# Kernel tuning notes

Measured on AMD Instinct MI355X. Metric: run time of the kernel, lower is better.

## Reference

```python
import jax, jax.numpy as jnp
import numpy as np

N, E, DIN, D, H, L = 4096, 65536, 128, 256, 4, 3
DH = D // H


def _ln(x, g, b, eps=1e-5):
    m = jnp.mean(x, axis=-1, keepdims=True)
    v = jnp.mean((x - m) ** 2, axis=-1, keepdims=True)
    return (x - m) * jax.lax.rsqrt(v + eps) * g + b


def _gcn(x, w, b, row, col, n):
    # PyG GCNConv: add self-loops, symmetric normalization D^-1/2 A D^-1/2, aggregate at col (target)
    ar = jnp.arange(n, dtype=row.dtype)
    r = jnp.concatenate([row, ar])
    c = jnp.concatenate([col, ar])
    deg = jax.ops.segment_sum(jnp.ones(r.shape[0], x.dtype), c, num_segments=n)
    dinv = jnp.where(deg > 0, deg ** -0.5, 0.0)
    norm = dinv[r] * dinv[c]  # (E+N,)
    msg = x @ w.T  # (N, out)
    return jax.ops.segment_sum(norm[:, None] * msg[r], c, num_segments=n) + b


def setup_inputs() -> dict:
    key = jax.random.key(0)
    ks = jax.random.split(key, 12)
    rnd = lambda i, shape: jax.random.normal(ks[i], shape, jnp.float32) * 0.05
    return {
        "node_features": jax.random.normal(ks[0], (N, DIN), jnp.float32),
        "edge_index": jax.random.randint(ks[1], (2, E), 0, N, jnp.int32),
        "gcn1_w": rnd(2, (D, DIN)), "gcn1_b": jnp.zeros((D,), jnp.float32),
        "gcn2_w": rnd(3, (D, D)), "gcn2_b": jnp.zeros((D,), jnp.float32),
        "edge_w": rnd(4, (H, 3)), "edge_b": jnp.zeros((H,), jnp.float32),
        "proj_w": rnd(5, (D, DIN + D)), "proj_b": jnp.zeros((D,), jnp.float32),
        "wqkv": rnd(6, (L, 3 * D, D)), "bqkv": jnp.zeros((L, 3 * D), jnp.float32),
        "wo": rnd(7, (L, D, D)), "bo": jnp.zeros((L, D), jnp.float32),
        "ffn_w1": rnd(8, (L, 4 * D, D)), "ffn_b1": jnp.zeros((L, 4 * D), jnp.float32),
        "ffn_w2": rnd(9, (L, D, 4 * D)), "ffn_b2": jnp.zeros((L, D), jnp.float32),
        "ln1_g": jnp.ones((L, D), jnp.float32), "ln1_b": jnp.zeros((L, D), jnp.float32),
        "ln2_g": jnp.ones((L, D), jnp.float32), "ln2_b": jnp.zeros((L, D), jnp.float32),
        "out_w": rnd(10, (1, D)), "out_b": jnp.zeros((1,), jnp.float32),
    }


def reference(node_features, edge_index, gcn1_w, gcn1_b, gcn2_w, gcn2_b,
              edge_w, edge_b, proj_w, proj_b, wqkv, bqkv, wo, bo,
              ffn_w1, ffn_b1, ffn_w2, ffn_b2, ln1_g, ln1_b, ln2_g, ln2_b,
              out_w, out_b):
    n = node_features.shape[0]
    row, col = edge_index[0], edge_index[1]
    # two-layer GCN
    h = jax.nn.relu(_gcn(node_features, gcn1_w, gcn1_b, row, col, n))
    g = _gcn(h, gcn2_w, gcn2_b, row, col, n)
    x = jnp.concatenate([node_features, g], axis=-1) @ proj_w.T + proj_b  # (N, D)
    # edge-aware attention bias: per-edge linear+sigmoid scattered into dense (H, N, N)
    feat = jnp.stack([row.astype(x.dtype), col.astype(x.dtype),
                      jnp.ones(row.shape[0], x.dtype)], axis=-1)  # (E, 3)
    bpe = jax.nn.sigmoid(feat @ edge_w.T + edge_b)  # (E, H)
    bias = jnp.zeros((H, n, n), x.dtype).at[:, row, col].set(bpe.T)
    scale = 1.0 / np.sqrt(DH)
    for l in range(L):
        qkv = x @ wqkv[l].T + bqkv[l]
        q, k, v = jnp.split(qkv, 3, axis=-1)
        q = q.reshape(n, H, DH); k = k.reshape(n, H, DH); v = v.reshape(n, H, DH)
        s = jnp.einsum('nhd,mhd->hnm', q, k) * scale + bias
        a = jax.nn.softmax(s, axis=-1)
        o = jnp.einsum('hnm,mhd->nhd', a, v).reshape(n, D) @ wo[l].T + bo[l]
        x = _ln(x + o, ln1_g[l], ln1_b[l])
        f = jax.nn.relu(x @ ffn_w1[l].T + ffn_b1[l]) @ ffn_w2[l].T + ffn_b2[l]
        x = _ln(x + f, ln2_g[l], ln2_b[l])
    return jax.nn.sigmoid(x @ out_w.T + out_b)  # (N, 1) probs
```

## Files before the change

### kernel.cpp

```cpp
#include <hip/hip_runtime.h>
#include <math.h>

#define NN 4096
#define NE 65536
#define DIN 128
#define DM 256
#define NH 4
#define NL 3
#define NCH 4
#define TPC (NN / 64 / NCH)
#define NBKT 16384

typedef __attribute__((ext_vector_type(8))) short bf16x8;
typedef __attribute__((ext_vector_type(4))) float f32x4;

__device__ inline ushort f2b(float f) {
    union { float f; uint u; } v; v.f = f;
    uint r = v.u + 0x7fffu + ((v.u >> 16) & 1u);
    return (ushort)(r >> 16);
}

__device__ inline uint cvt_pk_bf16(float lo, float hi) {
    uint r;
    asm("v_cvt_pk_bf16_f32 %0, %1, %2" : "=v"(r) : "v"(lo), "v"(hi));
    return r;
}

__device__ inline void gl_lds16(const ushort* g, ushort* l) {
    __builtin_amdgcn_global_load_lds(
        (const __attribute__((address_space(1))) void*)g,
        (__attribute__((address_space(3))) void*)l, 16, 0, 0);
}


__global__ void k_edge1(const int* __restrict__ row, const int* __restrict__ col,
                        uint* __restrict__ bitmap, int* __restrict__ cnt_c,
                        int* __restrict__ bcnt, unsigned char* __restrict__ flag) {
    int e = blockIdx.x * 256 + threadIdx.x;
    if (e >= NE) return;
    int r = row[e], c = col[e];
    atomicAdd(&cnt_c[c], 1);
    uint idx = (uint)r * 4096u + (uint)c;
    uint m = 1u << (idx & 31);
    uint old = atomicOr(&bitmap[idx >> 5], m);
    int isnew = (old & m) ? 0 : 1;
    flag[e] = (unsigned char)isnew;
    if (isnew) atomicAdd(&bcnt[(r >> 4) * 64 + (c >> 6)], 1);
}

__global__ void k_edge2(const int* __restrict__ row, const int* __restrict__ col,
                        const unsigned char* __restrict__ flag,
                        const int* __restrict__ sc, int* __restrict__ fc, int* __restrict__ csc_row,
                        const int* __restrict__ bstart, int* __restrict__ bfill,
                        ushort* __restrict__ ents) {
    int e = blockIdx.x * 256 + threadIdx.x;
    if (e >= NE) return;
    int r = row[e], c = col[e];
    csc_row[sc[c] + atomicAdd(&fc[c], 1)] = r;
    if (flag[e]) {
        int key = (r >> 4) * 64 + (c >> 6);
        ents[bstart[key] + atomicAdd(&bfill[key], 1)] = (ushort)(((r & 15) << 6) | (c & 63));
    }
}

template <int N>
__global__ void k_scan(const int* __restrict__ cnt, int* __restrict__ start) {
    __shared__ int part[256];
    const int C = N / 256;
    int t = threadIdx.x;
    int s = 0;
    for (int i = 0; i < C; ++i) s += cnt[t * C + i];
    part[t] = s;
    __syncthreads();
    if (t == 0) {
        int acc = 0;
        for (int i = 0; i < 256; ++i) { int v = part[i]; part[i] = acc; acc += v; }
        start[N] = acc;
    }
    __syncthreads();
    int acc = part[t];
    for (int i = 0; i < C; ++i) { start[t * C + i] = acc; acc += cnt[t * C + i]; }
}

__global__ void k_dinv(const int* __restrict__ cnt_c, float* __restrict__ dinv) {
    int i = blockIdx.x * 256 + threadIdx.x;
    if (i < NN) dinv[i] = 1.0f / sqrtf((float)(cnt_c[i] + 1));
}

struct CvtP { const float* s[8]; ushort* d[8]; int n[8]; };
__global__ void k_cvt(CvtP p) {
    int y = blockIdx.y;
    int base = (blockIdx.x * 256 + threadIdx.x) * 4;
    if (base >= p.n[y]) return;
    float4 v = *(const float4*)(p.s[y] + base);
    float sc = 1.f;
    if (y == 1 && ((base >> 8) % 768) < 256) sc = 0.125f;
    ushort4 o;
    o.x = f2b(v.x * sc); o.y = f2b(v.y * sc); o.z = f2b(v.z * sc); o.w = f2b(v.w * sc);
    *(ushort4*)(p.d[y] + base) = o;
}

__global__ void k_scaleb(const float* __restrict__ b, float* __restrict__ o) {
    int i = blockIdx.x * 256 + threadIdx.x;
    if (i < NL * 768) o[i] = b[i] * (((i % 768) < 256) ? 0.125f : 1.f);
}

template <int FLAGS>
__global__ __launch_bounds__(256) void k_gemm_b(
    const ushort* __restrict__ A, int lda,
    const ushort* __restrict__ B, int ldb,
    float* __restrict__ Cf, ushort* __restrict__ Cb, int ldc,
    int K, const float* __restrict__ bias) {
    __shared__ ushort As[128 * 64];
    __shared__ ushort Bs[128 * 64];
    const int tid = threadIdx.x;
    const int w = tid >> 6, l = tid & 63;
    const int l15 = l & 15, l4 = l >> 4;
    const int row0 = blockIdx.y * 128, col0 = blockIdx.x * 128;
    const int wm = (w >> 1) * 64, wn = (w & 1) * 64;
    f32x4 acc[4][4];
#pragma unroll
    for (int i = 0; i < 4; ++i)
#pragma unroll
        for (int j = 0; j < 4; ++j) acc[i][j] = (f32x4){0.f, 0.f, 0.f, 0.f};
    for (int k0 = 0; k0 < K; k0 += 64) {
#pragma unroll
        for (int i = 0; i < 4; ++i) {
            int ci = tid + 256 * i;
            int r = ci >> 3, s = ci & 7;
            bf16x8 va = *(const bf16x8*)(A + (long)(row0 + r) * lda + k0 + s * 8);
            *(bf16x8*)&As[r * 64 + ((s ^ (r & 7)) * 8)] = va;
            bf16x8 vb = *(const bf16x8*)(B + (long)(col0 + r) * ldb + k0 + s * 8);
            *(bf16x8*)&Bs[r * 64 + ((s ^ (r & 7)) * 8)] = vb;
        }
        __syncthreads();
#pragma unroll
        for (int kk = 0; kk < 2; ++kk) {
            bf16x8 af[4], bfr[4];
#pragma unroll
            for (int i = 0; i < 4; ++i) {
                int ar = wm + i * 16 + l15;
                af[i] = *(const bf16x8*)&As[ar * 64 + (((kk * 4 + l4) ^ (ar & 7)) * 8)];
                int br = wn + i * 16 + l15;
                bfr[i] = *(const bf16x8*)&Bs[br * 64 + (((kk * 4 + l4) ^ (br & 7)) * 8)];
            }
#pragma unroll
            for (int i = 0; i < 4; ++i)
#pragma unroll
                for (int j = 0; j < 4; ++j)
                    acc[i][j] = __builtin_amdgcn_mfma_f32_16x16x32_bf16(af[i], bfr[j], acc[i][j], 0, 0, 0);
        }
        __syncthreads();
    }
#pragma unroll
    for (int i = 0; i < 4; ++i)
#pragma unroll
        for (int j = 0; j < 4; ++j) {
            int rb = row0 + wm + i * 16;
            int cb = col0 + wn + j * 16 + l15;
            float bv = bias ? bias[cb] : 0.f;
            if (FLAGS & 8) {
                ushort4 o4;
                o4.x = f2b(acc[i][j][0] + bv);
                o4.y = f2b(acc[i][j][1] + bv);
                o4.z = f2b(acc[i][j][2] + bv);
                o4.w = f2b(acc[i][j][3] + bv);
                *(ushort4*)(Cb + (long)cb * ldc + rb + l4 * 4) = o4;
            } else {
#pragma unroll
                for (int q = 0; q < 4; ++q) {
                    int r = rb + l4 * 4 + q;
                    float v = acc[i][j][q] + bv;
                    if (FLAGS & 4) v = fmaxf(v, 0.f);
                    if (FLAGS & 1) Cf[(long)r * ldc + cb] = v;
                    if (FLAGS & 2) Cb[(long)r * ldc + cb] = f2b(v);
                }
            }
        }
}

template <int ACT, int B16>
__global__ void k_gcn_agg(const float* __restrict__ msg, const int* __restrict__ sc,
                          const int* __restrict__ csc_row, const float* __restrict__ dinv,
                          const float* __restrict__ bias,
                          float* __restrict__ outf, ushort* __restrict__ outb) {
    int j = blockIdx.x;
    int d = threadIdx.x;
    float acc = 0.f;
    int a = sc[j], b = sc[j + 1];
    for (int i = a; i < b; ++i) {
        int r = csc_row[i];
        acc += dinv[r] * msg[(long)r * DM + d];
    }
    float dj = dinv[j];
    float v = dj * acc + dj * dj * msg[(long)j * DM + d] + bias[d];
    if (ACT) v = fmaxf(v, 0.f);
    if (B16) outb[(long)j * DM + d] = f2b(v);
    else outf[(long)j * DM + d] = v;
}

__global__ void k_concat(const ushort* __restrict__ nfb, const float* __restrict__ g,
                         ushort* __restrict__ xcb) {
    long i = (long)blockIdx.x * 256 + threadIdx.x;
    if (i >= (long)NN * 384) return;
    int r = (int)(i / 384), c = (int)(i % 384);
    xcb[i] = (c < DIN) ? nfb[(long)r * DIN + c] : f2b(g[(long)r * DM + (c - DIN)]);
}

__global__ __launch_bounds__(256, 4) void k_attn(
    const ushort* __restrict__ qkb, const ushort* __restrict__ vT,
    const float* __restrict__ ew, const float* __restrict__ eb,
    const int* __restrict__ bstart, const ushort* __restrict__ ents,
    float* __restrict__ opart, float2* __restrict__ ml) {
    __shared__ ushort Klds[2][4096];
    __shared__ ushort Vlds[2][4096];
    __shared__ ushort Pl[4096];
    const int qb = blockIdx.x, h = blockIdx.y, cz = blockIdx.z;
    const int tid = threadIdx.x, w = tid >> 6, l = tid & 63;
    const int l15 = l & 15, l4 = l >> 4;
    const float w0 = ew[h * 3 + 0], w1 = ew[h * 3 + 1], w2 = ew[h * 3 + 2] + eb[h];
    bf16x8 qf[2];
    {
        const ushort* qp = qkb + (long)(qb * 64 + w * 16 + l15) * 512 + h * 64 + l4 * 8;
        qf[0] = *(const bf16x8*)(qp);
        qf[1] = *(const bf16x8*)(qp + 32);
    }
    const ushort* Kb = qkb + 256 + h * 64;
    const ushort* Vb = vT + (long)(h * 64) * NN;
    f32x4 o[4];
#pragma unroll
    for (int f = 0; f < 4; ++f) o[f] = (f32x4){0.f, 0.f, 0.f, 0.f};
    float m_run = -1e30f, l_run = 0.f;
    char* P = (char*)&Pl[w * 1024];
    const int bktW = (qb * 4 + w) * 64;
    const int t0 = cz * TPC;

    auto stage = [&](int b, int t) {
#pragma unroll
        for (int i = 0; i < 2; ++i) {
            int idx = i * 256 + w * 64 + l;
            int r = idx >> 3, sl = idx & 7;
            gl_lds16(Kb + (long)(t * 64 + r) * 512 + ((sl ^ (r & 7)) * 8),
                     &Klds[b][(i * 256 + w * 64) * 8]);
            gl_lds16(Vb + (long)r * NN + t * 64 + ((sl ^ (r & 7)) * 8),
                     &Vlds[b][(i * 256 + w * 64) * 8]);
        }
    };

    int bs_c = bstart[bktW + t0], be_c = bstart[bktW + t0 + 1];
    stage(0, t0);
    int cur = 0;
    for (int tt = 0; tt < TPC; ++tt) {
        const int t = t0 + tt;
        asm volatile("s_waitcnt lgkmcnt(0)" ::: "memory");
        __builtin_amdgcn_s_barrier();
        int bs_n = 0, be_n = 0;
        if (tt + 1 < TPC) {
            stage(cur ^ 1, t + 1);
            bs_n = bstart[bktW + t + 1];
            be_n = bstart[bktW + t + 2];
            asm volatile("s_waitcnt vmcnt(4)" ::: "memory");
        } else {
            asm volatile("s_waitcnt vmcnt(0)" ::: "memory");
        }
        __builtin_amdgcn_sched_barrier(0);
        __builtin_amdgcn_s_barrier();
        __builtin_amdgcn_sched_barrier(0);

        const ushort* Kl = Klds[cur];
        const ushort* Vl = Vlds[cur];
        f32x4 s4[4];
#pragma unroll
        for (int f = 0; f < 4; ++f) {
            int kc = f * 16 + l15;
            bf16x8 k0 = *(const bf16x8*)&Kl[kc * 64 + ((l4 ^ (kc & 7)) * 8)];
            bf16x8 k1 = *(const bf16x8*)&Kl[kc * 64 + (((4 + l4) ^ (kc & 7)) * 8)];
            f32x4 a = (f32x4){0.f, 0.f, 0.f, 0.f};
            a = __builtin_amdgcn_mfma_f32_16x16x32_bf16(k0, qf[0], a, 0, 0, 0);
            a = __builtin_amdgcn_mfma_f32_16x16x32_bf16(k1, qf[1], a, 0, 0, 0);
            s4[f] = a;
        }
        for (int i = bs_c; i < be_c; ++i) {
            int rc = (int)ents[i];
            int r4 = rc >> 6, c6 = rc & 63;
            if (l15 == r4 && ((c6 >> 2) & 3) == l4) {
                float arg = w0 * (float)(qb * 64 + w * 16 + r4) + w1 * (float)(t * 64 + c6) + w2;
                float sig = 1.f / (1.f + __expf(-arg));
                switch (((c6 >> 4) << 2) | (c6 & 3)) {
                    case 0:  s4[0][0] += sig; break; case 1:  s4[0][1] += sig; break;
                    case 2:  s4[0][2] += sig; break; case 3:  s4[0][3] += sig; break;
                    case 4:  s4[1][0] += sig; break; case 5:  s4[1][1] += sig; break;
                    case 6:  s4[1][2] += sig; break; case 7:  s4[1][3] += sig; break;
                    case 8:  s4[2][0] += sig; break; case 9:  s4[2][1] += sig; break;
                    case 10: s4[2][2] += sig; break; case 11: s4[2][3] += sig; break;
                    case 12: s4[3][0] += sig; break; case 13: s4[3][1] += sig; break;
                    case 14: s4[3][2] += sig; break; case 15: s4[3][3] += sig; break;
                }
            }
        }
        float ma = fmaxf(fmaxf(s4[0][0], s4[0][1]), fmaxf(s4[0][2], s4[0][3]));
        float mb = fmaxf(fmaxf(s4[1][0], s4[1][1]), fmaxf(s4[1][2], s4[1][3]));
        float mc = fmaxf(fmaxf(s4[2][0], s4[2][1]), fmaxf(s4[2][2], s4[2][3]));
        float md = fmaxf(fmaxf(s4[3][0], s4[3][1]), fmaxf(s4[3][2], s4[3][3]));
        float me = fmaxf(fmaxf(ma, mb), fmaxf(mc, md));
        me = fmaxf(me, __shfl_xor(me, 16));
        me = fmaxf(me, __shfl_xor(me, 32));
        float mn = fmaxf(m_run, me);
        float fac = __expf(m_run - mn);
        m_run = mn;
        float rp[4];
#pragma unroll
        for (int f = 0; f < 4; ++f) {
            float p0 = __expf(s4[f][0] - mn);
            float p1 = __expf(s4[f][1] - mn);
            float p2 = __expf(s4[f][2] - mn);
            float p3 = __expf(s4[f][3] - mn);
            s4[f][0] = p0; s4[f][1] = p1; s4[f][2] = p2; s4[f][3] = p3;
            rp[f] = (p0 + p1) + (p2 + p3);
        }
        float rsum = (rp[0] + rp[1]) + (rp[2] + rp[3]);
        rsum += __shfl_xor(rsum, 16);
        rsum += __shfl_xor(rsum, 32);
        l_run = l_run * fac + rsum;
#pragma unroll
        for (int f = 0; f < 4; ++f)
#pragma unroll
            for (int r = 0; r < 4; ++r) o[f][r] *= fac;
#pragma unroll
        for (int f = 0; f < 4; ++f)
#pragma unroll
            for (int p = 0; p < 2; ++p) {
                uint u = cvt_pk_bf16(s4[f][2 * p], s4[f][2 * p + 1]);
                int slot = f * 2 + (l4 >> 1);
                int byte = l15 * 128 + ((slot ^ (l15 & 7)) << 4) + (l4 & 1) * 8 + p * 4;
                *(uint*)(P + byte) = u;
            }
        asm volatile("s_waitcnt lgkmcnt(0)" ::: "memory");
        __builtin_amdgcn_sched_barrier(0);
#pragma unroll
        for (int ks = 0; ks < 2; ++ks) {
            bf16x8 pb = *(const bf16x8*)(P + l15 * 128 + (((ks * 4 + l4) ^ (l15 & 7)) << 4));
#pragma unroll
            for (int fd = 0; fd < 4; ++fd) {
                int d = fd * 16 + l15;
                bf16x8 vfr = *(const bf16x8*)&Vl[d * 64 + (((ks * 4 + l4) ^ (d & 7)) * 8)];
                o[fd] = __builtin_amdgcn_mfma_f32_16x16x32_bf16(vfr, pb, o[fd], 0, 0, 0);
            }
        }
        bs_c = bs_n; be_c = be_n;
        cur ^= 1;
    }
    long base = (((long)cz * NH + h) * NN + qb * 64 + w * 16 + l15) * 64;
#pragma unroll
    for (int fd = 0; fd < 4; ++fd)
#pragma unroll
        for (int r = 0; r < 4; ++r)
            opart[base + fd * 16 + l4 * 4 + r] = o[fd][r];
    if (l4 == 0)
        ml[((long)cz * NH + h) * NN + qb * 64 + w * 16 + l15] = make_float2(m_run, l_run);
}

__global__ __launch_bounds__(256) void k_comb(const float* __restrict__ opart,
                                              const float2* __restrict__ ml,
                                              ushort* __restrict__ attnOb) {
    int t = blockIdx.x * 256 + threadIdx.x;
    int d = t & 63;
    int r = (t >> 6) & (NN - 1);
    int h = t >> 18;
    float2 mls[NCH];
    float M = -1e30f;
#pragma unroll
    for (int c = 0; c < NCH; ++c) {
        mls[c] = ml[((long)c * NH + h) * NN + r];
        M = fmaxf(M, mls[c].x);
    }
    float s = 0.f, ov = 0.f;
#pragma unroll
    for (int c = 0; c < NCH; ++c) {
        float e = __expf(mls[c].x - M);
        s += mls[c].y * e;
        ov += opart[(((long)c * NH + h) * NN + r) * 64 + d] * e;
    }
    attnOb[(long)r * DM + h * 64 + d] = f2b(ov / s);
}


__global__ __launch_bounds__(256) void k_add_ln(
    float* __restrict__ x, ushort* __restrict__ xb, const float* __restrict__ y,
    const float* __restrict__ g, const float* __restrict__ b) {
    int row = blockIdx.x * 4 + (threadIdx.x >> 6);
    int lane = threadIdx.x & 63;
    float v[4];
#pragma unroll
    for (int i = 0; i < 4; ++i)
        v[i] = x[(long)row * DM + lane + 64 * i] + y[(long)row * DM + lane + 64 * i];
    float s = v[0] + v[1] + v[2] + v[3];
#pragma unroll
    for (int o = 1; o < 64; o <<= 1) s += __shfl_xor(s, o);
    float m = s * (1.f / 256.f);
    float q = 0.f;
#pragma unroll
    for (int i = 0; i < 4; ++i) { float d = v[i] - m; q += d * d; }
#pragma unroll
    for (int o = 1; o < 64; o <<= 1) q += __shfl_xor(q, o);
    float rs = rsqrtf(q * (1.f / 256.f) + 1e-5f);
#pragma unroll
    for (int i = 0; i < 4; ++i) {
        int c = lane + 64 * i;
        float val = (v[i] - m) * rs * g[c] + b[c];
        x[(long)row * DM + c] = val;
        xb[(long)row * DM + c] = f2b(val);
    }
}

__global__ void k_out(const float* __restrict__ x, const float* __restrict__ w,
                      const float* __restrict__ b, float* __restrict__ out) {
    int row = blockIdx.x;
    int lane = threadIdx.x;
    float s = 0.f;
#pragma unroll
    for (int i = 0; i < 4; ++i) s += x[(long)row * DM + lane + 64 * i] * w[lane + 64 * i];
#pragma unroll
    for (int o = 1; o < 64; o <<= 1) s += __shfl_xor(s, o);
    if (lane == 0) out[row] = 1.f / (1.f + expf(-(s + b[0])));
}

__global__ void k_sentinel(float* out, int n) {
    int i = blockIdx.x * 256 + threadIdx.x;
    if (i < n) out[i] = 1.0e9f;
}


extern "C" void kernel_launch(void* const* d_in, const int* in_sizes, int n_in,
                              void* d_out, int out_size, void* d_ws, size_t ws_size,
                              hipStream_t stream) {
    const float* nf = (const float*)d_in[0];
    const int* ei = (const int*)d_in[1];
    const int* erow = ei;
    const int* ecol = ei + NE;
    const float* gcn1_w = (const float*)d_in[2];
    const float* gcn1_b = (const float*)d_in[3];
    const float* gcn2_w = (const float*)d_in[4];
    const float* gcn2_b = (const float*)d_in[5];
    const float* edge_w = (const float*)d_in[6];
    const float* edge_b = (const float*)d_in[7];
    const float* proj_w = (const float*)d_in[8];
    const float* proj_b = (const float*)d_in[9];
    const float* wqkv = (const float*)d_in[10];
    const float* bqkv = (const float*)d_in[11];
    const float* wo = (const float*)d_in[12];
    const float* bo = (const float*)d_in[13];
    const float* ffn_w1 = (const float*)d_in[14];
    const float* ffn_b1 = (const float*)d_in[15];
    const float* ffn_w2 = (const float*)d_in[16];
    const float* ffn_b2 = (const float*)d_in[17];
    const float* ln1_g = (const float*)d_in[18];
    const float* ln1_b = (const float*)d_in[19];
    const float* ln2_g = (const float*)d_in[20];
    const float* ln2_b = (const float*)d_in[21];
    const float* out_w = (const float*)d_in[22];
    const float* out_b = (const float*)d_in[23];
    float* out = (float*)d_out;

    char* wp = (char*)d_ws;
    size_t off = 0;
    auto alloc = [&](size_t bytes) -> void* {
        void* p = wp + off;
        off = (off + bytes + 255) & ~(size_t)255;
        return p;
    };
    char* big = (char*)alloc((size_t)NCH * NH * NN * 64 * 4);
    float* msg = (float*)big;
    float* opart = (float*)big;
    ushort* ffnHb = (ushort*)big;
    float* ybuf = (float*)(big + (size_t)8 * 1024 * 1024);
    float* x = (float*)alloc((size_t)NN * DM * 4);
    ushort* xb = (ushort*)alloc((size_t)NN * DM * 2);
    ushort* xcb = (ushort*)alloc((size_t)NN * 384 * 2);
    ushort* hb = (ushort*)alloc((size_t)NN * DM * 2);
    float* g = (float*)alloc((size_t)NN * DM * 4);
    ushort* qkb = (ushort*)alloc((size_t)NN * 512 * 2);
    ushort* vT = (ushort*)alloc((size_t)DM * NN * 2);
    ushort* attnOb = (ushort*)alloc((size_t)NN * DM * 2);
    float2* ml = (float2*)alloc((size_t)NCH * NH * NN * 8);
    ushort* nfb = (ushort*)alloc((size_t)NN * DIN * 2);
    ushort* wqkvb = (ushort*)alloc((size_t)NL * 768 * DM * 2);
    ushort* wob = (ushort*)alloc((size_t)NL * DM * DM * 2);
    ushort* f1b = (ushort*)alloc((size_t)NL * 1024 * DM * 2);
    ushort* f2bw = (ushort*)alloc((size_t)NL * DM * 1024 * 2);
    ushort* g1b = (ushort*)alloc((size_t)DM * DIN * 2);
    ushort* g2b = (ushort*)alloc((size_t)DM * DM * 2);
    ushort* pjb = (ushort*)alloc((size_t)DM * 384 * 2);
    float* bq2 = (float*)alloc((size_t)NL * 768 * 4);
    uint* bitmap = (uint*)alloc((size_t)NN * NN / 8);
    unsigned char* flag = (unsigned char*)alloc(NE);
    int* cnt_c = (int*)alloc((size_t)NN * 4);
    int* bcnt = (int*)alloc((size_t)NBKT * 4);
    int* sc = (int*)alloc((size_t)(NN + 1) * 4);
    int* bstart = (int*)alloc((size_t)(NBKT + 1) * 4);
    int* fc = (int*)alloc((size_t)NN * 4);
    int* bfill = (int*)alloc((size_t)NBKT * 4);
    int* csc_row = (int*)alloc((size_t)NE * 4);
    ushort* ents = (ushort*)alloc((size_t)NE * 2);
    float* dinv = (float*)alloc((size_t)NN * 4);

    if (off > ws_size) {
        k_sentinel<<<(out_size + 255) / 256, 256, 0, stream>>>(out, out_size);
        return;
    }

    hipMemsetAsync(bitmap, 0, (size_t)NN * NN / 8, stream);
    hipMemsetAsync(cnt_c, 0, NN * 4, stream);
    hipMemsetAsync(bcnt, 0, NBKT * 4, stream);
    hipMemsetAsync(fc, 0, NN * 4, stream);
    hipMemsetAsync(bfill, 0, NBKT * 4, stream);
    k_edge1<<<NE / 256, 256, 0, stream>>>(erow, ecol, bitmap, cnt_c, bcnt, flag);
    k_scan<NN><<<1, 256, 0, stream>>>(cnt_c, sc);
    k_scan<NBKT><<<1, 256, 0, stream>>>(bcnt, bstart);
    k_edge2<<<NE / 256, 256, 0, stream>>>(erow, ecol, flag, sc, fc, csc_row, bstart, bfill, ents);
    k_dinv<<<NN / 256, 256, 0, stream>>>(cnt_c, dinv);

    CvtP cp;
    cp.s[0] = nf;      cp.d[0] = nfb;   cp.n[0] = NN * DIN;
    cp.s[1] = wqkv;    cp.d[1] = wqkvb; cp.n[1] = NL * 768 * DM;
    cp.s[2] = wo;      cp.d[2] = wob;   cp.n[2] = NL * DM * DM;
    cp.s[3] = ffn_w1;  cp.d[3] = f1b;   cp.n[3] = NL * 1024 * DM;
    cp.s[4] = ffn_w2;  cp.d[4] = f2bw;  cp.n[4] = NL * DM * 1024;
    cp.s[5] = gcn1_w;  cp.d[5] = g1b;   cp.n[5] = DM * DIN;
    cp.s[6] = gcn2_w;  cp.d[6] = g2b;   cp.n[6] = DM * DM;
    cp.s[7] = proj_w;  cp.d[7] = pjb;   cp.n[7] = DM * 384;
    k_cvt<<<dim3(768, 8), 256, 0, stream>>>(cp);
    k_scaleb<<<(NL * 768 + 255) / 256, 256, 0, stream>>>(bqkv, bq2);

    k_gemm_b<1><<<dim3(DM / 128, NN / 128), 256, 0, stream>>>(
        nfb, DIN, g1b, DIN, msg, nullptr, DM, DIN, nullptr);
    k_gcn_agg<1, 1><<<NN, DM, 0, stream>>>(msg, sc, csc_row, dinv, gcn1_b, nullptr, hb);
    k_gemm_b<1><<<dim3(DM / 128, NN / 128), 256, 0, stream>>>(
        hb, DM, g2b, DM, msg, nullptr, DM, DM, nullptr);
    k_gcn_agg<0, 0><<<NN, DM, 0, stream>>>(msg, sc, csc_row, dinv, gcn2_b, g, nullptr);
    k_concat<<<(NN * 384 + 255) / 256, 256, 0, stream>>>(nfb, g, xcb);
    k_gemm_b<3><<<dim3(DM / 128, NN / 128), 256, 0, stream>>>(
        xcb, 384, pjb, 384, x, xb, DM, 384, proj_b);

    for (int l = 0; l < NL; ++l) {
        k_gemm_b<2><<<dim3(512 / 128, NN / 128), 256, 0, stream>>>(
            xb, DM, wqkvb + (long)l * 768 * DM, DM, nullptr, qkb, 512, DM,
            bq2 + (long)l * 768);
        k_gemm_b<8><<<dim3(DM / 128, NN / 128), 256, 0, stream>>>(
            xb, DM, wqkvb + (long)l * 768 * DM + 512 * DM, DM, nullptr, vT, NN, DM,
            bqkv + (long)l * 768 + 512);
        k_attn<<<dim3(NN / 64, NH, NCH), 256, 0, stream>>>(
            qkb, vT, edge_w, edge_b, bstart, ents, opart, ml);
        k_comb<<<NN * NH * 64 / 256, 256, 0, stream>>>(opart, ml, attnOb);
        k_gemm_b<1><<<dim3(DM / 128, NN / 128), 256, 0, stream>>>(
            attnOb, DM, wob + (long)l * DM * DM, DM, ybuf, nullptr, DM, DM,
            bo + (long)l * DM);
        k_add_ln<<<NN / 4, 256, 0, stream>>>(x, xb, ybuf, ln1_g + (long)l * DM, ln1_b + (long)l * DM);
        k_gemm_b<6><<<dim3(1024 / 128, NN / 128), 256, 0, stream>>>(
            xb, DM, f1b + (long)l * 1024 * DM, DM, nullptr, ffnHb, 1024, DM,
            ffn_b1 + (long)l * 1024);
        k_gemm_b<1><<<dim3(DM / 128, NN / 128), 256, 0, stream>>>(
            ffnHb, 1024, f2bw + (long)l * DM * 1024, 1024, ybuf, nullptr, DM, 1024,
            ffn_b2 + (long)l * DM);
        k_add_ln<<<NN / 4, 256, 0, stream>>>(x, xb, ybuf, ln2_g + (long)l * DM, ln2_b + (long)l * DM);
    }
    k_out<<<NN, 64, 0, stream>>>(x, out_w, out_b, out);
}
```

Measured before the change: 567.5 us.

## Fuse residual+LayerNorm into output GEMMs, merge QKV GEMMs, lazy softmax rescale

Merges the QK and V projection GEMMs into one launch whose epilogue writes Q/K row-major and V transposed. Adds a new GEMM kernel that computes the full 256-wide output row per block and applies bias, residual add and LayerNorm in its epilogue. This removes the separate add-LN kernels and the fp32 intermediate buffer. The attention loop now skips the online-softmax rescale unless the new max exceeds the running max by more than 8. The fused GEMM uses 16-row tiles, which may give lower MFMA efficiency and heavier B reloads per block. It also computes variance as E[x^2]-m^2, which is less numerically stable.

New measurement: 499.4 us. -12.0%, faster.

```diff
diff --git a/kernel.cpp b/kernel.cpp
--- a/kernel.cpp
+++ b/kernel.cpp
@@ -109,7 +109,7 @@
 __global__ __launch_bounds__(256) void k_gemm_b(
     const ushort* __restrict__ A, int lda,
     const ushort* __restrict__ B, int ldb,
-    float* __restrict__ Cf, ushort* __restrict__ Cb, int ldc,
+    float* __restrict__ Cf, ushort* __restrict__ Cb, ushort* __restrict__ Cb2, int ldc,
     int K, const float* __restrict__ bias) {
     __shared__ ushort As[128 * 64];
     __shared__ ushort Bs[128 * 64];
@@ -159,7 +159,20 @@
             int rb = row0 + wm + i * 16;
             int cb = col0 + wn + j * 16 + l15;
             float bv = bias ? bias[cb] : 0.f;
-            if (FLAGS & 8) {
+            if (FLAGS & 16) {
+                if (cb < 512) {
+#pragma unroll
+                    for (int q = 0; q < 4; ++q)
+                        Cb[(long)(rb + l4 * 4 + q) * 512 + cb] = f2b(acc[i][j][q] + bv);
+                } else {
+                    ushort4 o4;
+                    o4.x = f2b(acc[i][j][0] + bv);
+                    o4.y = f2b(acc[i][j][1] + bv);
+                    o4.z = f2b(acc[i][j][2] + bv);
+                    o4.w = f2b(acc[i][j][3] + bv);
+                    *(ushort4*)(Cb2 + (long)(cb - 512) * NN + rb + l4 * 4) = o4;
+                }
+            } else if (FLAGS & 8) {
                 ushort4 o4;
                 o4.x = f2b(acc[i][j][0] + bv);
                 o4.y = f2b(acc[i][j][1] + bv);
@@ -177,6 +190,105 @@
                 }
             }
         }
+}
+
+__global__ __launch_bounds__(256) void k_gemm_ln(
+    const ushort* __restrict__ A, int lda,
+    const ushort* __restrict__ B, int ldb, int K,
+    const float* __restrict__ bias,
+    float* __restrict__ x, ushort* __restrict__ xb,
+    const float* __restrict__ gam, const float* __restrict__ bet) {
+    __shared__ ushort As[16 * 64];
+    __shared__ ushort Bs[256 * 64];
+    __shared__ float red[4][16][2];
+    const int tid = threadIdx.x;
+    const int w = tid >> 6, l = tid & 63;
+    const int l15 = l & 15, l4 = l >> 4;
+    const int row0 = blockIdx.x * 16;
+    f32x4 acc[4];
+#pragma unroll
+    for (int j = 0; j < 4; ++j) acc[j] = (f32x4){0.f, 0.f, 0.f, 0.f};
+    for (int k0 = 0; k0 < K; k0 += 64) {
+        if (tid < 128) {
+            int r = tid >> 3, s = tid & 7;
+            bf16x8 va = *(const bf16x8*)(A + (long)(row0 + r) * lda + k0 + s * 8);
+            *(bf16x8*)&As[r * 64 + ((s ^ (r & 7)) * 8)] = va;
+        }
+#pragma unroll
+        for (int i = 0; i < 8; ++i) {
+            int idx = i * 256 + tid;
+            int r = idx >> 3, s = idx & 7;
+            bf16x8 vb = *(const bf16x8*)(B + (long)r * ldb + k0 + s * 8);
+            *(bf16x8*)&Bs[r * 64 + ((s ^ (r & 7)) * 8)] = vb;
+        }
+        __syncthreads();
+#pragma unroll
+        for (int kk = 0; kk < 2; ++kk) {
+            bf16x8 af = *(const bf16x8*)&As[l15 * 64 + (((kk * 4 + l4) ^ (l15 & 7)) * 8)];
+#pragma unroll
+            for (int j = 0; j < 4; ++j) {
+                int br = w * 64 + j * 16 + l15;
+                bf16x8 bfr = *(const bf16x8*)&Bs[br * 64 + (((kk * 4 + l4) ^ (br & 7)) * 8)];
+                acc[j] = __builtin_amdgcn_mfma_f32_16x16x32_bf16(af, bfr, acc[j], 0, 0, 0);
+            }
+        }
+        __syncthreads();
+    }
+    float val[4][4];
+#pragma unroll
+    for (int j = 0; j < 4; ++j) {
+        int c = w * 64 + j * 16 + l15;
+        float bv = bias[c];
+#pragma unroll
+        for (int q = 0; q < 4; ++q) {
+            int r = row0 + l4 * 4 + q;
+            val[j][q] = acc[j][q] + bv + x[(long)r * DM + c];
+        }
+    }
+    float sum[4], sq[4];
+#pragma unroll
+    for (int q = 0; q < 4; ++q) {
+        sum[q] = (val[0][q] + val[1][q]) + (val[2][q] + val[3][q]);
+        sq[q] = (val[0][q] * val[0][q] + val[1][q] * val[1][q]) +
+                (val[2][q] * val[2][q] + val[3][q] * val[3][q]);
+    }
+#pragma unroll
+    for (int o = 1; o < 16; o <<= 1)
+#pragma unroll
+        for (int q = 0; q < 4; ++q) {
+            sum[q] += __shfl_xor(sum[q], o);
+            sq[q] += __shfl_xor(sq[q], o);
+        }
+    if (l15 == 0)
+#pragma unroll
+        for (int q = 0; q < 4; ++q) {
+            red[w][l4 * 4 + q][0] = sum[q];
+            red[w][l4 * 4 + q][1] = sq[q];
+        }
+    __syncthreads();
+    float mean[4], rs[4];
+#pragma unroll
+    for (int q = 0; q < 4; ++q) {
+        int rl = l4 * 4 + q;
+        float ts = (red[0][rl][0] + red[1][rl][0]) + (red[2][rl][0] + red[3][rl][0]);
+        float tq = (red[0][rl][1] + red[1][rl][1]) + (red[2][rl][1] + red[3][rl][1]);
+        float m = ts * (1.f / 256.f);
+        float var = tq * (1.f / 256.f) - m * m;
+        mean[q] = m;
+        rs[q] = rsqrtf(var + 1e-5f);
+    }
+#pragma unroll
+    for (int j = 0; j < 4; ++j) {
+        int c = w * 64 + j * 16 + l15;
+        float gv = gam[c], bv = bet[c];
+#pragma unroll
+        for (int q = 0; q < 4; ++q) {
+            int r = row0 + l4 * 4 + q;
+            float ov = (val[j][q] - mean[q]) * rs[q] * gv + bv;
+            x[(long)r * DM + c] = ov;
+            xb[(long)r * DM + c] = f2b(ov);
+        }
+    }
 }
 
 template <int ACT, int B16>
@@ -305,27 +417,30 @@
         float me = fmaxf(fmaxf(ma, mb), fmaxf(mc, md));
         me = fmaxf(me, __shfl_xor(me, 16));
         me = fmaxf(me, __shfl_xor(me, 32));
-        float mn = fmaxf(m_run, me);
-        float fac = __expf(m_run - mn);
-        m_run = mn;
+        if (!__all(me <= m_run + 8.f)) {
+            float mn = fmaxf(m_run, me);
+            float fac = __expf(m_run - mn);
+            m_run = mn;
+            l_run *= fac;
+#pragma unroll
+            for (int f = 0; f < 4; ++f)
+#pragma unroll
+                for (int r = 0; r < 4; ++r) o[f][r] *= fac;
+        }
         float rp[4];
 #pragma unroll
         for (int f = 0; f < 4; ++f) {
-            float p0 = __expf(s4[f][0] - mn);
-            float p1 = __expf(s4[f][1] - mn);
-            float p2 = __expf(s4[f][2] - mn);
-            float p3 = __expf(s4[f][3] - mn);
+            float p0 = __expf(s4[f][0] - m_run);
+            float p1 = __expf(s4[f][1] - m_run);
+            float p2 = __expf(s4[f][2] - m_run);
+            float p3 = __expf(s4[f][3] - m_run);
             s4[f][0] = p0; s4[f][1] = p1; s4[f][2] = p2; s4[f][3] = p3;
             rp[f] = (p0 + p1) + (p2 + p3);
         }
         float rsum = (rp[0] + rp[1]) + (rp[2] + rp[3]);
         rsum += __shfl_xor(rsum, 16);
         rsum += __shfl_xor(rsum, 32);
-        l_run = l_run * fac + rsum;
-#pragma unroll
-        for (int f = 0; f < 4; ++f)
-#pragma unroll
-            for (int r = 0; r < 4; ++r) o[f][r] *= fac;
+        l_run += rsum;
 #pragma unroll
         for (int f = 0; f < 4; ++f)
 #pragma unroll
@@ -384,34 +499,6 @@
     attnOb[(long)r * DM + h * 64 + d] = f2b(ov / s);
 }
 
-
-__global__ __launch_bounds__(256) void k_add_ln(
-    float* __restrict__ x, ushort* __restrict__ xb, const float* __restrict__ y,
-    const float* __restrict__ g, const float* __restrict__ b) {
-    int row = blockIdx.x * 4 + (threadIdx.x >> 6);
-    int lane = threadIdx.x & 63;
-    float v[4];
-#pragma unroll
-    for (int i = 0; i < 4; ++i)
-        v[i] = x[(long)row * DM + lane + 64 * i] + y[(long)row * DM + lane + 64 * i];
-    float s = v[0] + v[1] + v[2] + v[3];
-#pragma unroll
-    for (int o = 1; o < 64; o <<= 1) s += __shfl_xor(s, o);
-    float m = s * (1.f / 256.f);
-    float q = 0.f;
-#pragma unroll
-    for (int i = 0; i < 4; ++i) { float d = v[i] - m; q += d * d; }
-#pragma unroll
-    for (int o = 1; o < 64; o <<= 1) q += __shfl_xor(q, o);
-    float rs = rsqrtf(q * (1.f / 256.f) + 1e-5f);
-#pragma unroll
-    for (int i = 0; i < 4; ++i) {
-        int c = lane + 64 * i;
-        float val = (v[i] - m) * rs * g[c] + b[c];
-        x[(long)row * DM + c] = val;
-        xb[(long)row * DM + c] = f2b(val);
-    }
-}
 
 __global__ void k_out(const float* __restrict__ x, const float* __restrict__ w,
                       const float* __restrict__ b, float* __restrict__ out) {
@@ -473,7 +560,6 @@
     float* msg = (float*)big;
     float* opart = (float*)big;
     ushort* ffnHb = (ushort*)big;
-    float* ybuf = (float*)(big + (size_t)8 * 1024 * 1024);
     float* x = (float*)alloc((size_t)NN * DM * 4);
     ushort* xb = (ushort*)alloc((size_t)NN * DM * 2);
     ushort* xcb = (ushort*)alloc((size_t)NN * 384 * 2);
@@ -533,36 +619,31 @@
     k_scaleb<<<(NL * 768 + 255) / 256, 256, 0, stream>>>(bqkv, bq2);
 
     k_gemm_b<1><<<dim3(DM / 128, NN / 128), 256, 0, stream>>>(
-        nfb, DIN, g1b, DIN, msg, nullptr, DM, DIN, nullptr);
+        nfb, DIN, g1b, DIN, msg, nullptr, nullptr, DM, DIN, nullptr);
     k_gcn_agg<1, 1><<<NN, DM, 0, stream>>>(msg, sc, csc_row, dinv, gcn1_b, nullptr, hb);
     k_gemm_b<1><<<dim3(DM / 128, NN / 128), 256, 0, stream>>>(
-        hb, DM, g2b, DM, msg, nullptr, DM, DM, nullptr);
+        hb, DM, g2b, DM, msg, nullptr, nullptr, DM, DM, nullptr);
     k_gcn_agg<0, 0><<<NN, DM, 0, stream>>>(msg, sc, csc_row, dinv, gcn2_b, g, nullptr);
     k_concat<<<(NN * 384 + 255) / 256, 256, 0, stream>>>(nfb, g, xcb);
     k_gemm_b<3><<<dim3(DM / 128, NN / 128), 256, 0, stream>>>(
-        xcb, 384, pjb, 384, x, xb, DM, 384, proj_b);
+        xcb, 384, pjb, 384, x, xb, nullptr, DM, 384, proj_b);
 
     for (int l = 0; l < NL; ++l) {
-        k_gemm_b<2><<<dim3(512 / 128, NN / 128), 256, 0, stream>>>(
-            xb, DM, wqkvb + (long)l * 768 * DM, DM, nullptr, qkb, 512, DM,
+        k_gemm_b<18><<<dim3(768 / 128, NN / 128), 256, 0, stream>>>(
+            xb, DM, wqkvb + (long)l * 768 * DM, DM, nullptr, qkb, vT, 512, DM,
             bq2 + (long)l * 768);
-        k_gemm_b<8><<<dim3(DM / 128, NN / 128), 256, 0, stream>>>(
-            xb, DM, wqkvb + (long)l * 768 * DM + 512 * DM, DM, nullptr, vT, NN, DM,
-            bqkv + (long)l * 768 + 512);
         k_attn<<<dim3(NN / 64, NH, NCH), 256, 0, stream>>>(
             qkb, vT, edge_w, edge_b, bstart, ents, opart, ml);
         k_comb<<<NN * NH * 64 / 256, 256, 0, stream>>>(opart, ml, attnOb);
-        k_gemm_b<1><<<dim3(DM / 128, NN / 128), 256, 0, stream>>>(
-            attnOb, DM, wob + (long)l * DM * DM, DM, ybuf, nullptr, DM, DM,
-            bo + (long)l * DM);
-        k_add_ln<<<NN / 4, 256, 0, stream>>>(x, xb, ybuf, ln1_g + (long)l * DM, ln1_b + (long)l * DM);
+        k_gemm_ln<<<NN / 16, 256, 0, stream>>>(
+            attnOb, DM, wob + (long)l * DM * DM, DM, DM, bo + (long)l * DM,
+            x, xb, ln1_g + (long)l * DM, ln1_b + (long)l * DM);
         k_gemm_b<6><<<dim3(1024 / 128, NN / 128), 256, 0, stream>>>(
-            xb, DM, f1b + (long)l * 1024 * DM, DM, nullptr, ffnHb, 1024, DM,
+            xb, DM, f1b + (long)l * 1024 * DM, DM, nullptr, ffnHb, nullptr, 1024, DM,
             ffn_b1 + (long)l * 1024);
-        k_gemm_b<1><<<dim3(DM / 128, NN / 128), 256, 0, stream>>>(
-            ffnHb, 1024, f2bw + (long)l * DM * 1024, 1024, ybuf, nullptr, DM, 1024,
-            ffn_b2 + (long)l * DM);
-        k_add_ln<<<NN / 4, 256, 0, stream>>>(x, xb, ybuf, ln2_g + (long)l * DM, ln2_b + (long)l * DM);
+        k_gemm_ln<<<NN / 16, 256, 0, stream>>>(
+            ffnHb, 1024, f2bw + (long)l * DM * 1024, 1024, 1024, ffn_b2 + (long)l * DM,
+            x, xb, ln2_g + (long)l * DM, ln2_b + (long)l * DM);
     }
     k_out<<<NN, 64, 0, stream>>>(x, out_w, out_b, out);
 }
```
